# Kernel tuning notes

Hardware: AMD Instinct MI355X
Metric: run time of the kernel (lower is better)

The kernel has to match this reference:

```python
import jax, jax.numpy as jnp
import numpy as np

# Dims: B samples, D=2048 backbone feature dim (resnet50 fc.in_features),
B, D, G, R, K, C = 16384, 2048, 8, 6, 3, 16


def setup_inputs() -> dict:
    key = jax.random.key(0)
    k0, k1, k2, k3 = jax.random.split(key, 4)
    feats = jax.random.normal(k0, (B, D), dtype=jnp.float32)          # backbone output (dropout=eval identity)
    roi_ids = jax.random.randint(k1, (B,), 0, G)                       # per-sample routing id (roi_names)
    W_reg = jax.random.normal(k2, (G, R, D), dtype=jnp.float32) * 0.02  # reg_heads[roi].weight
    b_reg = jnp.zeros((G, R), dtype=jnp.float32)                       # reg_heads[roi].bias
    W_cls = jax.random.normal(k3, (G, K, C, D), dtype=jnp.float32) * 0.02  # cls_heads[roi][k].weight
    b_cls = jnp.zeros((G, K, C), dtype=jnp.float32)                    # cls_heads[roi][k].bias
    return {"feats": feats, "roi_ids": roi_ids, "W_reg": W_reg, "b_reg": b_reg,
            "W_cls": W_cls, "b_cls": b_cls}


def reference(feats, roi_ids, W_reg, b_reg, W_cls, b_cls):
    # Original loop applies, per sample i, the Linear heads of roi_names[i].
    # Vectorized: compute all-ROI head outputs densely, then gather the routed one.
    # (Same math per sample; dropout is identity in eval mode.)
    reg_all = jnp.einsum('bd,grd->bgr', feats, W_reg) + b_reg[None]        # [B, G, R]
    cls_all = jnp.einsum('bd,gkcd->bgkc', feats, W_cls) + b_cls[None]      # [B, G, K, C]
    reg = jnp.take_along_axis(reg_all, roi_ids[:, None, None], axis=1)[:, 0]            # [B, R]
    cls = jnp.take_along_axis(cls_all, roi_ids[:, None, None, None], axis=1)[:, 0]      # [B, K, C]
    return reg, cls
```

## Files before the change

### kernel.cpp

```cpp
#include <hip/hip_runtime.h>
#include <hip/hip_bf16.h>

#define NB   16384
#define ND   2048
#define NG   8
#define NR   6
#define NKC  48
#define NOUT 54
#define BM   32
#define KC3  64
#define NCH3 (ND / KC3)
#define SLOT 16384
#define LROW 136
#define KC   128
#define NCH  (ND / KC)
#define MAXT (NB / BM + NG)

typedef __attribute__((ext_vector_type(8))) short short8_t;
typedef __attribute__((ext_vector_type(4))) float f32x4;

__device__ __forceinline__ unsigned short f2bf(float x) {
    union { float f; unsigned u; } v; v.f = x;
    unsigned r = v.u + 0x7FFFu + ((v.u >> 16) & 1u);
    return (unsigned short)(r >> 16);
}

__device__ __forceinline__ short8_t cvt8(float4 a, float4 b) {
    short8_t s;
    s[0] = (short)f2bf(a.x); s[1] = (short)f2bf(a.y);
    s[2] = (short)f2bf(a.z); s[3] = (short)f2bf(a.w);
    s[4] = (short)f2bf(b.x); s[5] = (short)f2bf(b.y);
    s[6] = (short)f2bf(b.z); s[7] = (short)f2bf(b.w);
    return s;
}

__device__ __forceinline__ void gl_lds16(const void* g, void* s) {
    __builtin_amdgcn_global_load_lds(
        (const __attribute__((address_space(1))) void*)g,
        (__attribute__((address_space(3))) void*)s,
        16, 0, 0);
}

#define WAITV(N) do { asm volatile("s_waitcnt vmcnt(" #N ")" ::: "memory"); \
                      __builtin_amdgcn_sched_barrier(0); } while (0)
#define BARRIER() do { __builtin_amdgcn_s_barrier(); \
                       __builtin_amdgcn_sched_barrier(0); } while (0)

__global__ void hist_kernel(const int* __restrict__ roi, int* __restrict__ counts) {
    int i = blockIdx.x * 256 + threadIdx.x;
    int g = roi[i];
    int lane = threadIdx.x & 63;
    #pragma unroll
    for (int gg = 0; gg < NG; ++gg) {
        unsigned long long m = __ballot(g == gg);
        if (m && lane == (int)(__ffsll((unsigned long long)m) - 1))
            atomicAdd(&counts[gg], (int)__popcll(m));
    }
}

__global__ void scatter_kernel(const int* __restrict__ roi, const int* __restrict__ counts,
                               int* __restrict__ ranks, int* __restrict__ perm) {
    int off[NG];
    int acc = 0;
    #pragma unroll
    for (int gg = 0; gg < NG; ++gg) { off[gg] = acc; acc += counts[gg]; }
    int i = blockIdx.x * 256 + threadIdx.x;
    int g = roi[i];
    int lane = threadIdx.x & 63;
    #pragma unroll
    for (int gg = 0; gg < NG; ++gg) {
        unsigned long long m = __ballot(g == gg);
        if (!m) continue;
        int leader = (int)(__ffsll((unsigned long long)m) - 1);
        int base = 0;
        if (lane == leader) base = atomicAdd(&ranks[gg], (int)__popcll(m));
        base = __shfl(base, leader);
        if (g == gg) {
            int rank = (int)__popcll(m & ((1ull << lane) - 1ull));
            perm[off[gg] + base + rank] = i;
        }
    }
}

__global__ void scatter1_kernel(const int* __restrict__ roi, int* __restrict__ cnt,
                                int* __restrict__ perm) {
    int i = blockIdx.x * 256 + threadIdx.x;
    int g = roi[i];
    int lane = threadIdx.x & 63;
    #pragma unroll
    for (int gg = 0; gg < NG; ++gg) {
        unsigned long long m = __ballot(g == gg);
        if (!m) continue;
        int leader = (int)(__ffsll((unsigned long long)m) - 1);
        int base = 0;
        if (lane == leader) base = atomicAdd(&cnt[gg], (int)__popcll(m));
        base = __shfl(base, leader);
        if (g == gg) {
            int rank = (int)__popcll(m & ((1ull << lane) - 1ull));
            perm[gg * NB + base + rank] = i;
        }
    }
}

__global__ void wconv_kernel(const float* __restrict__ Wreg, const float* __restrict__ Wcls,
                             short* __restrict__ Wbf) {
    int u = blockIdx.x * 256 + threadIdx.x;
    int l  = u & 63;
    int ks = (u >> 6) & 1;
    int n  = (u >> 7) & 1;
    int nh = (u >> 8) & 1;
    int c  = (u >> 9) & 31;
    int g  = u >> 14;
    int row = nh * 32 + n * 16 + (l & 15);
    int k   = c * 64 + ks * 32 + (l >> 4) * 8;
    short8_t v = {0, 0, 0, 0, 0, 0, 0, 0};
    if (row < NOUT) {
        const float* s = (row < NR) ? Wreg + (size_t)(g * NR + row) * ND + k
                                    : Wcls + (size_t)(g * NKC + row - NR) * ND + k;
        float4 a = *(const float4*)s;
        float4 b = *(const float4*)(s + 4);
        v = cvt8(a, b);
    }
    *(short8_t*)(Wbf + (size_t)u * 8) = v;
}

__launch_bounds__(256, 2)
__global__ void gemm_p3_kernel(const float* __restrict__ feats,
                               const short* __restrict__ Wbf,
                               const float* __restrict__ breg, const float* __restrict__ bcls,
                               const int* __restrict__ counts, const int* __restrict__ perm,
                               float* __restrict__ out, int stride) {
    __shared__ __align__(16) char lds[3][SLOT];
    __shared__ int sRow[BM];

    int ts[NG + 1]; ts[0] = 0;
    int off[NG]; int acc_ = 0;
    #pragma unroll
    for (int gg = 0; gg < NG; ++gg) {
        int c = counts[gg];
        off[gg] = stride ? gg * stride : acc_;
        acc_ += c;
        ts[gg + 1] = ts[gg] + (c + BM - 1) / BM;
    }
    int b = blockIdx.x;
    if (b >= ts[NG]) return;
    int g = 0;
    #pragma unroll
    for (int gg = 0; gg < NG; ++gg) if (b >= ts[gg + 1]) g = gg + 1;
    int gcnt  = counts[g];
    int goff  = off[g];
    int rbase = (b - ts[g]) * BM;
    int nvalid = gcnt - rbase; if (nvalid > BM) nvalid = BM;

    int tid = threadIdx.x;
    if (tid < BM) {
        int r = rbase + tid;
        if (r >= gcnt) r = gcnt - 1;
        sRow[tid] = perm[goff + r];
    }
    __syncthreads();

    int w = tid >> 6, l = tid & 63, lr = l & 15, lq = l >> 4;
    int mt = w & 1, nh = w >> 1;

    const float* paBase = feats + (size_t)sRow[mt * 16 + lr] * ND + nh * 32 + lq * 8;
    char* ldsA = &lds[0][0] + (mt * 4096 + nh * 2048);
    const short* pbBase = Wbf + ((size_t)g * 32 * 8 + (nh * 2 + mt) * 2) * 512 + l * 8;
    char* ldsB = &lds[0][8192] + (nh * 4096 + mt * 2048);

#define STAGE(cc, sl) do {                                                     \
        const float* a_ = paBase + (size_t)(cc) * KC3;                         \
        gl_lds16(a_,     ldsA + (sl) * SLOT);                                  \
        gl_lds16(a_ + 4, ldsA + (sl) * SLOT + 1024);                           \
        const short* b_ = pbBase + (size_t)(cc) * 4096;                        \
        gl_lds16(b_,       ldsB + (sl) * SLOT);                                \
        gl_lds16(b_ + 512, ldsB + (sl) * SLOT + 1024);                         \
    } while (0)

    f32x4 acc0 = {0, 0, 0, 0}, acc1 = {0, 0, 0, 0};

    STAGE(0, 0); STAGE(1, 1);

    #pragma unroll
    for (int c = 0; c < NCH3; ++c) {
        const int sl = c % 3;
        if (c + 2 < NCH3) STAGE(c + 2, (c + 2) % 3);
        if (c < NCH3 - 2)       WAITV(8);
        else if (c == NCH3 - 2) WAITV(4);
        else                    WAITV(0);
        BARRIER();
        {
            const char* sa = &lds[sl][mt * 4096];
            const char* sb = &lds[sl][8192 + nh * 4096];
            #pragma unroll
            for (int ks = 0; ks < 2; ++ks) {
                float4 a0 = *(const float4*)(sa + ks * 2048 + l * 16);
                float4 a1 = *(const float4*)(sa + ks * 2048 + 1024 + l * 16);
                short8_t af = cvt8(a0, a1);
                short8_t b0 = *(const short8_t*)(sb + ks * 1024 + l * 16);
                short8_t b1 = *(const short8_t*)(sb + 2048 + ks * 1024 + l * 16);
                acc0 = __builtin_amdgcn_mfma_f32_16x16x32_bf16(af, b0, acc0, 0, 0, 0);
                acc1 = __builtin_amdgcn_mfma_f32_16x16x32_bf16(af, b1, acc1, 0, 0, 0);
            }
        }
        BARRIER();
    }
#undef STAGE

    const int B6 = NB * NR;
    #pragma unroll
    for (int n = 0; n < 2; ++n) {
        f32x4 v = n ? acc1 : acc0;
        int col = nh * 32 + n * 16 + lr;
        if (col < NOUT) {
            #pragma unroll
            for (int j = 0; j < 4; ++j) {
                int row = mt * 16 + lq * 4 + j;
                if (row < nvalid) {
                    int smp = sRow[row];
                    if (col < NR) out[smp * NR + col] = v[j] + breg[g * NR + col];
                    else          out[B6 + smp * NKC + (col - NR)] = v[j] + bcls[g * NKC + (col - NR)];
                }
            }
        }
    }
}

__launch_bounds__(256, 3)
__global__ void gemm_kernel(const float* __restrict__ feats,
                            const float* __restrict__ Wreg, const float* __restrict__ breg,
                            const float* __restrict__ Wcls, const float* __restrict__ bcls,
                            const int* __restrict__ counts, const int* __restrict__ perm,
                            float* __restrict__ out, int stride) {
    __shared__ __align__(16) short Bsh[2][64][LROW];
    __shared__ int sRow[BM];

    int ts[NG + 1]; ts[0] = 0;
    int off[NG]; int acc = 0;
    #pragma unroll
    for (int gg = 0; gg < NG; ++gg) {
        int c = counts[gg];
        off[gg] = stride ? gg * stride : acc;
        acc += c;
        ts[gg + 1] = ts[gg] + (c + BM - 1) / BM;
    }
    int b = blockIdx.x;
    if (b >= ts[NG]) return;
    int g = 0;
    #pragma unroll
    for (int gg = 0; gg < NG; ++gg) if (b >= ts[gg + 1]) g = gg + 1;
    int gcnt  = counts[g];
    int goff  = off[g];
    int rbase = (b - ts[g]) * BM;
    int nvalid = gcnt - rbase; if (nvalid > BM) nvalid = BM;

    int tid = threadIdx.x;
    if (tid < BM) {
        int r = rbase + tid;
        if (r >= gcnt) r = gcnt - 1;
        sRow[tid] = perm[goff + r];
    }
    __syncthreads();

    int rB = tid >> 2;
    int cq = tid & 3;
    const float* wsrc = nullptr;
    if (rB < NR)        wsrc = Wreg + ((size_t)g * NR + rB) * ND + cq * 32;
    else if (rB < NOUT) wsrc = Wcls + ((size_t)g * NKC + (rB - NR)) * ND + cq * 32;

    int w = tid >> 6, l = tid & 63, lr = l & 15, lq = l >> 4;
    int mt = w & 1, nh = w >> 1;
    const float* aptr = feats + (size_t)sRow[mt * 16 + lr] * ND + lq * 8;
    const short* brp = (const short*)&Bsh[0][0][0] + (nh * 32 + lr) * LROW + lq * 8;

    f32x4 acc0 = {0, 0, 0, 0}, acc1 = {0, 0, 0, 0};
    float4 rb[8];

    if (wsrc) {
        #pragma unroll
        for (int i = 0; i < 8; ++i) rb[i] = *(const float4*)(wsrc + 4 * i);
    } else {
        #pragma unroll
        for (int i = 0; i < 8; ++i) rb[i] = make_float4(0.f, 0.f, 0.f, 0.f);
    }
    {
        short* bw = &Bsh[0][rB][cq * 32];
        #pragma unroll
        for (int j = 0; j < 4; ++j) *(short8_t*)(bw + 8 * j) = cvt8(rb[2 * j], rb[2 * j + 1]);
    }
    __syncthreads();

    #pragma unroll
    for (int c = 0; c < NCH; ++c) {
        const int cur = c & 1, nxt = cur ^ 1;
        if (c + 1 < NCH && wsrc) {
            const float* s = wsrc + (c + 1) * KC;
            #pragma unroll
            for (int i = 0; i < 8; ++i) rb[i] = *(const float4*)(s + 4 * i);
        }
        const short* bp = brp + cur * (64 * LROW);
        const float* ap = aptr + c * KC;
        #pragma unroll
        for (int ks = 0; ks < 4; ++ks) {
            float4 a0 = *(const float4*)(ap + ks * 32);
            float4 a1 = *(const float4*)(ap + ks * 32 + 4);
            short8_t af = cvt8(a0, a1);
            short8_t b0 = *(const short8_t*)(bp + ks * 32);
            short8_t b1 = *(const short8_t*)(bp + 16 * LROW + ks * 32);
            acc0 = __builtin_amdgcn_mfma_f32_16x16x32_bf16(af, b0, acc0, 0, 0, 0);
            acc1 = __builtin_amdgcn_mfma_f32_16x16x32_bf16(af, b1, acc1, 0, 0, 0);
        }
        if (c + 1 < NCH && wsrc) {
            short* bw = &Bsh[nxt][rB][cq * 32];
            #pragma unroll
            for (int j = 0; j < 4; ++j) *(short8_t*)(bw + 8 * j) = cvt8(rb[2 * j], rb[2 * j + 1]);
        } else if (c + 1 < NCH) {
            short8_t z = {0,0,0,0,0,0,0,0};
            short* bw = &Bsh[nxt][rB][cq * 32];
            #pragma unroll
            for (int j = 0; j < 4; ++j) *(short8_t*)(bw + 8 * j) = z;
        }
        __syncthreads();
    }

    const int B6 = NB * NR;
    #pragma unroll
    for (int n = 0; n < 2; ++n) {
        f32x4 v = n ? acc1 : acc0;
        int col = nh * 32 + n * 16 + lr;
        if (col < NOUT) {
            #pragma unroll
            for (int j = 0; j < 4; ++j) {
                int row = mt * 16 + lq * 4 + j;
                if (row < nvalid) {
                    int smp = sRow[row];
                    if (col < NR) out[smp * NR + col] = v[j] + breg[g * NR + col];
                    else          out[B6 + smp * NKC + (col - NR)] = v[j] + bcls[g * NKC + (col - NR)];
                }
            }
        }
    }
}

__global__ void fallback_kernel(const float* __restrict__ feats, const int* __restrict__ roi,
                                const float* __restrict__ Wreg, const float* __restrict__ breg,
                                const float* __restrict__ Wcls, const float* __restrict__ bcls,
                                float* __restrict__ out) {
    int i = blockIdx.x;
    int lane = threadIdx.x;
    int g = roi[i];
    const float* frow = feats + (size_t)i * ND;
    float f[32];
    #pragma unroll
    for (int q = 0; q < 32; ++q) f[q] = frow[lane + 64 * q];
    for (int o = 0; o < NOUT; ++o) {
        const float* wrow = (o < NR) ? Wreg + ((size_t)g * NR + o) * ND
                                     : Wcls + ((size_t)g * NKC + (o - NR)) * ND;
        float p = 0.f;
        #pragma unroll
        for (int q = 0; q < 32; ++q) p += f[q] * wrow[lane + 64 * q];
        #pragma unroll
        for (int s = 32; s; s >>= 1) p += __shfl_xor(p, s);
        if (lane == 0) {
            if (o < NR) out[i * NR + o] = p + breg[g * NR + o];
            else        out[NB * NR + i * NKC + (o - NR)] = p + bcls[g * NKC + (o - NR)];
        }
    }
}

extern "C" void kernel_launch(void* const* d_in, const int* in_sizes, int n_in,
                              void* d_out, int out_size, void* d_ws, size_t ws_size,
                              hipStream_t stream) {
    const float* feats = (const float*)d_in[0];
    const int*   roi   = (const int*)d_in[1];
    const float* Wreg  = (const float*)d_in[2];
    const float* breg  = (const float*)d_in[3];
    const float* Wcls  = (const float*)d_in[4];
    const float* bcls  = (const float*)d_in[5];
    float* out = (float*)d_out;

    const size_t wbfBytes = (size_t)NG * 131072 * 2;
    const size_t need_t1 = wbfBytes + 256 + (size_t)NG * NB * 4;
    const size_t need_t3 = 256 + (size_t)NB * 4;

    if (ws_size >= need_t1) {
        short* Wbf = (short*)d_ws;
        int* cnt  = (int*)((char*)d_ws + wbfBytes);
        int* perm = cnt + 64;
        hipMemsetAsync(cnt, 0, 8 * sizeof(int), stream);
        wconv_kernel<<<512, 256, 0, stream>>>(Wreg, Wcls, Wbf);
        scatter1_kernel<<<NB / 256, 256, 0, stream>>>(roi, cnt, perm);
        gemm_p3_kernel<<<MAXT, 256, 0, stream>>>(feats, Wbf, breg, bcls, cnt, perm, out, NB);
    } else if (ws_size >= need_t3) {
        int* counts = (int*)d_ws;
        int* ranks  = counts + 8;
        int* perm   = counts + 64;
        hipMemsetAsync(counts, 0, 16 * sizeof(int), stream);
        hist_kernel<<<NB / 256, 256, 0, stream>>>(roi, counts);
        scatter_kernel<<<NB / 256, 256, 0, stream>>>(roi, counts, ranks, perm);
        gemm_kernel<<<MAXT, 256, 0, stream>>>(feats, Wreg, breg, Wcls, bcls, counts, perm, out, 0);
    } else {
        fallback_kernel<<<NB, 64, 0, stream>>>(feats, roi, Wreg, breg, Wcls, bcls, out);
    }
}
```

Before: 69.91 us.

## Fuse prep kernels and use persistent work-queue GEMM with 64-row tiles

Merges the routing scatter and weight bf16 conversion into one prep kernel, cutting one launch. Replaces the per-tile GEMM grid with a persistent 512-block kernel of 512 threads. Each block pulls 64-row tiles from an atomic queue head and stages A through XOR-swizzled LDS to avoid bank conflicts. This aims to reduce launch overhead and tail imbalance and to improve reuse of the B tile, at the cost of larger LDS use and an atomic per tile.

```diff
diff --git a/kernel.cpp b/kernel.cpp
--- a/kernel.cpp
+++ b/kernel.cpp
@@ -7,11 +7,8 @@
 #define NR   6
 #define NKC  48
 #define NOUT 54
+#define LROW 136
 #define BM   32
-#define KC3  64
-#define NCH3 (ND / KC3)
-#define SLOT 16384
-#define LROW 136
 #define KC   128
 #define NCH  (ND / KC)
 #define MAXT (NB / BM + NG)
@@ -43,8 +40,8 @@
 
 #define WAITV(N) do { asm volatile("s_waitcnt vmcnt(" #N ")" ::: "memory"); \
                       __builtin_amdgcn_sched_barrier(0); } while (0)
-#define BARRIER() do { __builtin_amdgcn_s_barrier(); \
-                       __builtin_amdgcn_sched_barrier(0); } while (0)
+#define BAR() do { __builtin_amdgcn_s_barrier(); \
+                   __builtin_amdgcn_sched_barrier(0); } while (0)
 
 __global__ void hist_kernel(const int* __restrict__ roi, int* __restrict__ counts) {
     int i = blockIdx.x * 256 + threadIdx.x;
@@ -82,64 +79,176 @@
     }
 }
 
-__global__ void scatter1_kernel(const int* __restrict__ roi, int* __restrict__ cnt,
-                                int* __restrict__ perm) {
-    int i = blockIdx.x * 256 + threadIdx.x;
-    int g = roi[i];
-    int lane = threadIdx.x & 63;
-    #pragma unroll
-    for (int gg = 0; gg < NG; ++gg) {
-        unsigned long long m = __ballot(g == gg);
-        if (!m) continue;
-        int leader = (int)(__ffsll((unsigned long long)m) - 1);
-        int base = 0;
-        if (lane == leader) base = atomicAdd(&cnt[gg], (int)__popcll(m));
-        base = __shfl(base, leader);
-        if (g == gg) {
-            int rank = (int)__popcll(m & ((1ull << lane) - 1ull));
-            perm[gg * NB + base + rank] = i;
-        }
-    }
-}
-
-__global__ void wconv_kernel(const float* __restrict__ Wreg, const float* __restrict__ Wcls,
-                             short* __restrict__ Wbf) {
-    int u = blockIdx.x * 256 + threadIdx.x;
-    int l  = u & 63;
-    int ks = (u >> 6) & 1;
-    int n  = (u >> 7) & 1;
-    int nh = (u >> 8) & 1;
-    int c  = (u >> 9) & 31;
-    int g  = u >> 14;
-    int row = nh * 32 + n * 16 + (l & 15);
-    int k   = c * 64 + ks * 32 + (l >> 4) * 8;
-    short8_t v = {0, 0, 0, 0, 0, 0, 0, 0};
-    if (row < NOUT) {
-        const float* s = (row < NR) ? Wreg + (size_t)(g * NR + row) * ND + k
-                                    : Wcls + (size_t)(g * NKC + row - NR) * ND + k;
-        float4 a = *(const float4*)s;
-        float4 b = *(const float4*)(s + 4);
-        v = cvt8(a, b);
-    }
-    *(short8_t*)(Wbf + (size_t)u * 8) = v;
-}
-
-__launch_bounds__(256, 2)
-__global__ void gemm_p3_kernel(const float* __restrict__ feats,
-                               const short* __restrict__ Wbf,
-                               const float* __restrict__ breg, const float* __restrict__ bcls,
-                               const int* __restrict__ counts, const int* __restrict__ perm,
-                               float* __restrict__ out, int stride) {
-    __shared__ __align__(16) char lds[3][SLOT];
+__global__ void prep_kernel(const int* __restrict__ roi, int* __restrict__ cnt,
+                            int* __restrict__ perm,
+                            const float* __restrict__ Wreg, const float* __restrict__ Wcls,
+                            short* __restrict__ Wbf) {
+    if (blockIdx.x < 64) {
+        int i = blockIdx.x * 256 + threadIdx.x;
+        int g = roi[i];
+        int lane = threadIdx.x & 63;
+        #pragma unroll
+        for (int gg = 0; gg < NG; ++gg) {
+            unsigned long long m = __ballot(g == gg);
+            if (!m) continue;
+            int leader = (int)(__ffsll((unsigned long long)m) - 1);
+            int base = 0;
+            if (lane == leader) base = atomicAdd(&cnt[gg], (int)__popcll(m));
+            base = __shfl(base, leader);
+            if (g == gg) {
+                int rank = (int)__popcll(m & ((1ull << lane) - 1ull));
+                perm[gg * NB + base + rank] = i;
+            }
+        }
+    } else {
+        int u = (blockIdx.x - 64) * 256 + threadIdx.x;
+        int l = u & 63;
+        int q = (u >> 6) & 7;
+        int c = (u >> 9) & 31;
+        int g = u >> 14;
+        int nh = q >> 2, nf = (q >> 1) & 1, ks = q & 1;
+        int row = nh * 32 + nf * 16 + (l & 15);
+        int k   = c * 64 + ks * 32 + (l >> 4) * 8;
+        short8_t v = {0, 0, 0, 0, 0, 0, 0, 0};
+        if (row < NOUT) {
+            const float* s = (row < NR) ? Wreg + (size_t)(g * NR + row) * ND + k
+                                        : Wcls + (size_t)(g * NKC + row - NR) * ND + k;
+            float4 a = *(const float4*)s;
+            float4 b = *(const float4*)(s + 4);
+            v = cvt8(a, b);
+        }
+        *(short8_t*)(Wbf + (size_t)u * 8) = v;
+    }
+}
+
+__launch_bounds__(512, 4)
+__global__ void gemm_q_kernel(const float* __restrict__ feats,
+                              const short* __restrict__ Wbf,
+                              const float* __restrict__ breg, const float* __restrict__ bcls,
+                              const int* __restrict__ cnt, const int* __restrict__ perm,
+                              int* __restrict__ qhead, float* __restrict__ out) {
+    __shared__ __align__(16) char lds[3][24576];
+    __shared__ int sRow[64];
+    __shared__ int sTile;
+
+    int tid = threadIdx.x, w = tid >> 6, l = tid & 63, lr = l & 15, lq = l >> 4;
+    int mt = w >> 1, nh = w & 1;
+
+    int ts[NG + 1]; ts[0] = 0;
+    #pragma unroll
+    for (int gg = 0; gg < NG; ++gg) ts[gg + 1] = ts[gg] + ((cnt[gg] + 63) >> 6);
+    const int Ttot = ts[NG];
+
+    const int key   = lr & 7;
+    const int rbyt  = mt * 4096 + lr * 256;
+    const int o00 = (((lq * 2 + 0) ^ key) << 4);
+    const int o01 = (((lq * 2 + 1) ^ key) << 4);
+    const int o10 = (((8 + lq * 2 + 0) ^ key) << 4);
+    const int o11 = (((8 + lq * 2 + 1) ^ key) << 4);
+    const int r0 = (2 * w + 0) * 4 + lq;
+    const int r1 = (2 * w + 1) * 4 + lq;
+    const int sp0 = (((l & 15) ^ (r0 & 7)) << 4);
+    const int sp1 = (((l & 15) ^ (r1 & 7)) << 4);
+    const int B6 = NB * NR;
+
+    for (;;) {
+        if (tid == 0) sTile = atomicAdd(qhead, 1);
+        __syncthreads();
+        int t = sTile;
+        if (t >= Ttot) break;
+
+        int g = 0;
+        #pragma unroll
+        for (int gg = 0; gg < NG; ++gg) if (t >= ts[gg + 1]) g = gg + 1;
+        int cg = cnt[g];
+        int rbase = (t - ts[g]) * 64;
+        int nv = cg - rbase; if (nv > 64) nv = 64;
+
+        if (tid < 64) {
+            int r = rbase + tid;
+            if (r >= cg) r = cg - 1;
+            sRow[tid] = perm[g * NB + r];
+        }
+        __syncthreads();
+
+        const char* a0c = (const char*)(feats + (size_t)sRow[r0] * ND) + sp0;
+        const char* a1c = (const char*)(feats + (size_t)sRow[r1] * ND) + sp1;
+        const char* bB  = (const char*)Wbf + (size_t)g * 262144 + w * 1024 + l * 16;
+
+#define STAGE(cc, sl) do {                                                     \
+        size_t co_ = (size_t)(cc) * 256;                                       \
+        gl_lds16(a0c + co_, &lds[sl][w * 2048]);                               \
+        gl_lds16(a1c + co_, &lds[sl][w * 2048 + 1024]);                        \
+        gl_lds16(bB + (size_t)(cc) * 8192, &lds[sl][16384 + w * 1024]);        \
+    } while (0)
+
+#define CSTEP(ks, o_0, o_1) do {                                               \
+        const char* Ab_ = &lds[csl][0] + rbyt;                                 \
+        const char* Bb_ = &lds[csl][16384] + nh * 4096 + (ks) * 1024 + l * 16; \
+        float4 x0 = *(const float4*)(Ab_ + (ks) * 0 + o_0);                    \
+        float4 x1 = *(const float4*)(Ab_ + o_1);                               \
+        short8_t af = cvt8(x0, x1);                                            \
+        short8_t b0 = *(const short8_t*)(Bb_);                                 \
+        short8_t b1 = *(const short8_t*)(Bb_ + 2048);                          \
+        acc0 = __builtin_amdgcn_mfma_f32_16x16x32_bf16(af, b0, acc0, 0, 0, 0); \
+        acc1 = __builtin_amdgcn_mfma_f32_16x16x32_bf16(af, b1, acc1, 0, 0, 0); \
+    } while (0)
+
+        f32x4 acc0 = {0, 0, 0, 0}, acc1 = {0, 0, 0, 0};
+
+        STAGE(0, 0); STAGE(1, 1);
+        int csl = 0;
+        #pragma unroll
+        for (int c = 0; c < 32; ++c) {
+            if (c + 2 < 32) STAGE(c + 2, (c + 2) % 3);
+            if (c < 30)       WAITV(6);
+            else if (c == 30) WAITV(3);
+            else              WAITV(0);
+            BAR();
+            CSTEP(0, o00, o01);
+            CSTEP(1, o10, o11);
+            BAR();
+            csl = (csl == 2) ? 0 : csl + 1;
+        }
+#undef STAGE
+#undef CSTEP
+
+        #pragma unroll
+        for (int n = 0; n < 2; ++n) {
+            f32x4 v = n ? acc1 : acc0;
+            int col = nh * 32 + n * 16 + lr;
+            if (col < NOUT) {
+                #pragma unroll
+                for (int j = 0; j < 4; ++j) {
+                    int row = mt * 16 + lq * 4 + j;
+                    if (row < nv) {
+                        int smp = sRow[row];
+                        if (col < NR) out[smp * NR + col] = v[j] + breg[g * NR + col];
+                        else          out[B6 + smp * NKC + (col - NR)] = v[j] + bcls[g * NKC + (col - NR)];
+                    }
+                }
+            }
+        }
+        __syncthreads();
+    }
+}
+
+__launch_bounds__(256, 3)
+__global__ void gemm_kernel(const float* __restrict__ feats,
+                            const float* __restrict__ Wreg, const float* __restrict__ breg,
+                            const float* __restrict__ Wcls, const float* __restrict__ bcls,
+                            const int* __restrict__ counts, const int* __restrict__ perm,
+                            float* __restrict__ out, int stride) {
+    __shared__ __align__(16) short Bsh[2][64][LROW];
     __shared__ int sRow[BM];
 
     int ts[NG + 1]; ts[0] = 0;
-    int off[NG]; int acc_ = 0;
+    int off[NG]; int acc = 0;
     #pragma unroll
     for (int gg = 0; gg < NG; ++gg) {
         int c = counts[gg];
-        off[gg] = stride ? gg * stride : acc_;
-        acc_ += c;
+        off[gg] = stride ? gg * stride : acc;
+        acc += c;
         ts[gg + 1] = ts[gg] + (c + BM - 1) / BM;
     }
     int b = blockIdx.x;
@@ -160,52 +269,66 @@
     }
     __syncthreads();
 
+    int rB = tid >> 2;
+    int cq = tid & 3;
+    const float* wsrc = nullptr;
+    if (rB < NR)        wsrc = Wreg + ((size_t)g * NR + rB) * ND + cq * 32;
+    else if (rB < NOUT) wsrc = Wcls + ((size_t)g * NKC + (rB - NR)) * ND + cq * 32;
+
     int w = tid >> 6, l = tid & 63, lr = l & 15, lq = l >> 4;
     int mt = w & 1, nh = w >> 1;
-
-    const float* paBase = feats + (size_t)sRow[mt * 16 + lr] * ND + nh * 32 + lq * 8;
-    char* ldsA = &lds[0][0] + (mt * 4096 + nh * 2048);
-    const short* pbBase = Wbf + ((size_t)g * 32 * 8 + (nh * 2 + mt) * 2) * 512 + l * 8;
-    char* ldsB = &lds[0][8192] + (nh * 4096 + mt * 2048);
-
-#define STAGE(cc, sl) do {                                                     \
-        const float* a_ = paBase + (size_t)(cc) * KC3;                         \
-        gl_lds16(a_,     ldsA + (sl) * SLOT);                                  \
-        gl_lds16(a_ + 4, ldsA + (sl) * SLOT + 1024);                           \
-        const short* b_ = pbBase + (size_t)(cc) * 4096;                        \
-        gl_lds16(b_,       ldsB + (sl) * SLOT);                                \
-        gl_lds16(b_ + 512, ldsB + (sl) * SLOT + 1024);                         \
-    } while (0)
+    const float* aptr = feats + (size_t)sRow[mt * 16 + lr] * ND + lq * 8;
+    const short* brp = (const short*)&Bsh[0][0][0] + (nh * 32 + lr) * LROW + lq * 8;
 
     f32x4 acc0 = {0, 0, 0, 0}, acc1 = {0, 0, 0, 0};
-
-    STAGE(0, 0); STAGE(1, 1);
-
-    #pragma unroll
-    for (int c = 0; c < NCH3; ++c) {
-        const int sl = c % 3;
-        if (c + 2 < NCH3) STAGE(c + 2, (c + 2) % 3);
-        if (c < NCH3 - 2)       WAITV(8);
-        else if (c == NCH3 - 2) WAITV(4);
-        else                    WAITV(0);
-        BARRIER();
-        {
-            const char* sa = &lds[sl][mt * 4096];
-            const char* sb = &lds[sl][8192 + nh * 4096];
+    float4 rb[8];
+
+    if (wsrc) {
+        #pragma unroll
+        for (int i = 0; i < 8; ++i) rb[i] = *(const float4*)(wsrc + 4 * i);
+    } else {
+        #pragma unroll
+        for (int i = 0; i < 8; ++i) rb[i] = make_float4(0.f, 0.f, 0.f, 0.f);
+    }
+    {
+        short* bw = &Bsh[0][rB][cq * 32];
+        #pragma unroll
+        for (int j = 0; j < 4; ++j) *(short8_t*)(bw + 8 * j) = cvt8(rb[2 * j], rb[2 * j + 1]);
+    }
+    __syncthreads();
+
+    #pragma unroll
+    for (int c = 0; c < NCH; ++c) {
+        const int cur = c & 1, nxt = cur ^ 1;
+        if (c + 1 < NCH && wsrc) {
+            const float* s = wsrc + (c + 1) * KC;
             #pragma unroll
-            for (int ks = 0; ks < 2; ++ks) {
-                float4 a0 = *(const float4*)(sa + ks * 2048 + l * 16);
-                float4 a1 = *(const float4*)(sa + ks * 2048 + 1024 + l * 16);
-                short8_t af = cvt8(a0, a1);
-                short8_t b0 = *(const short8_t*)(sb + ks * 1024 + l * 16);
-                short8_t b1 = *(const short8_t*)(sb + 2048 + ks * 1024 + l * 16);
-                acc0 = __builtin_amdgcn_mfma_f32_16x16x32_bf16(af, b0, acc0, 0, 0, 0);
-                acc1 = __builtin_amdgcn_mfma_f32_16x16x32_bf16(af, b1, acc1, 0, 0, 0);
-            }
-        }
-        BARRIER();
-    }
-#undef STAGE
+            for (int i = 0; i < 8; ++i) rb[i] = *(const float4*)(s + 4 * i);
+        }
+        const short* bp = brp + cur * (64 * LROW);
+        const float* ap = aptr + c * KC;
+        #pragma unroll
+        for (int ks = 0; ks < 4; ++ks) {
+            float4 a0 = *(const float4*)(ap + ks * 32);
+            float4 a1 = *(const float4*)(ap + ks * 32 + 4);
+            short8_t af = cvt8(a0, a1);
+            short8_t b0 = *(const short8_t*)(bp + ks * 32);
+            short8_t b1 = *(const short8_t*)(bp + 16 * LROW + ks * 32);
+            acc0 = __builtin_amdgcn_mfma_f32_16x16x32_bf16(af, b0, acc0, 0, 0, 0);
+            acc1 = __builtin_amdgcn_mfma_f32_16x16x32_bf16(af, b1, acc1, 0, 0, 0);
+        }
+        if (c + 1 < NCH && wsrc) {
+            short* bw = &Bsh[nxt][rB][cq * 32];
+            #pragma unroll
+            for (int j = 0; j < 4; ++j) *(short8_t*)(bw + 8 * j) = cvt8(rb[2 * j], rb[2 * j + 1]);
+        } else if (c + 1 < NCH) {
+            short8_t z = {0,0,0,0,0,0,0,0};
+            short* bw = &Bsh[nxt][rB][cq * 32];
+            #pragma unroll
+            for (int j = 0; j < 4; ++j) *(short8_t*)(bw + 8 * j) = z;
+        }
+        __syncthreads();
+    }
 
     const int B6 = NB * NR;
     #pragma unroll
@@ -226,122 +349,6 @@
     }
 }
 
-__launch_bounds__(256, 3)
-__global__ void gemm_kernel(const float* __restrict__ feats,
-                            const float* __restrict__ Wreg, const float* __restrict__ breg,
-                            const float* __restrict__ Wcls, const float* __restrict__ bcls,
-                            const int* __restrict__ counts, const int* __restrict__ perm,
-                            float* __restrict__ out, int stride) {
-    __shared__ __align__(16) short Bsh[2][64][LROW];
-    __shared__ int sRow[BM];
-
-    int ts[NG + 1]; ts[0] = 0;
-    int off[NG]; int acc = 0;
-    #pragma unroll
-    for (int gg = 0; gg < NG; ++gg) {
-        int c = counts[gg];
-        off[gg] = stride ? gg * stride : acc;
-        acc += c;
-        ts[gg + 1] = ts[gg] + (c + BM - 1) / BM;
-    }
-    int b = blockIdx.x;
-    if (b >= ts[NG]) return;
-    int g = 0;
-    #pragma unroll
-    for (int gg = 0; gg < NG; ++gg) if (b >= ts[gg + 1]) g = gg + 1;
-    int gcnt  = counts[g];
-    int goff  = off[g];
-    int rbase = (b - ts[g]) * BM;
-    int nvalid = gcnt - rbase; if (nvalid > BM) nvalid = BM;
-
-    int tid = threadIdx.x;
-    if (tid < BM) {
-        int r = rbase + tid;
-        if (r >= gcnt) r = gcnt - 1;
-        sRow[tid] = perm[goff + r];
-    }
-    __syncthreads();
-
-    int rB = tid >> 2;
-    int cq = tid & 3;
-    const float* wsrc = nullptr;
-    if (rB < NR)        wsrc = Wreg + ((size_t)g * NR + rB) * ND + cq * 32;
-    else if (rB < NOUT) wsrc = Wcls + ((size_t)g * NKC + (rB - NR)) * ND + cq * 32;
-
-    int w = tid >> 6, l = tid & 63, lr = l & 15, lq = l >> 4;
-    int mt = w & 1, nh = w >> 1;
-    const float* aptr = feats + (size_t)sRow[mt * 16 + lr] * ND + lq * 8;
-    const short* brp = (const short*)&Bsh[0][0][0] + (nh * 32 + lr) * LROW + lq * 8;
-
-    f32x4 acc0 = {0, 0, 0, 0}, acc1 = {0, 0, 0, 0};
-    float4 rb[8];
-
-    if (wsrc) {
-        #pragma unroll
-        for (int i = 0; i < 8; ++i) rb[i] = *(const float4*)(wsrc + 4 * i);
-    } else {
-        #pragma unroll
-        for (int i = 0; i < 8; ++i) rb[i] = make_float4(0.f, 0.f, 0.f, 0.f);
-    }
-    {
-        short* bw = &Bsh[0][rB][cq * 32];
-        #pragma unroll
-        for (int j = 0; j < 4; ++j) *(short8_t*)(bw + 8 * j) = cvt8(rb[2 * j], rb[2 * j + 1]);
-    }
-    __syncthreads();
-
-    #pragma unroll
-    for (int c = 0; c < NCH; ++c) {
-        const int cur = c & 1, nxt = cur ^ 1;
-        if (c + 1 < NCH && wsrc) {
-            const float* s = wsrc + (c + 1) * KC;
-            #pragma unroll
-            for (int i = 0; i < 8; ++i) rb[i] = *(const float4*)(s + 4 * i);
-        }
-        const short* bp = brp + cur * (64 * LROW);
-        const float* ap = aptr + c * KC;
-        #pragma unroll
-        for (int ks = 0; ks < 4; ++ks) {
-            float4 a0 = *(const float4*)(ap + ks * 32);
-            float4 a1 = *(const float4*)(ap + ks * 32 + 4);
-            short8_t af = cvt8(a0, a1);
-            short8_t b0 = *(const short8_t*)(bp + ks * 32);
-            short8_t b1 = *(const short8_t*)(bp + 16 * LROW + ks * 32);
-            acc0 = __builtin_amdgcn_mfma_f32_16x16x32_bf16(af, b0, acc0, 0, 0, 0);
-            acc1 = __builtin_amdgcn_mfma_f32_16x16x32_bf16(af, b1, acc1, 0, 0, 0);
-        }
-        if (c + 1 < NCH && wsrc) {
-            short* bw = &Bsh[nxt][rB][cq * 32];
-            #pragma unroll
-            for (int j = 0; j < 4; ++j) *(short8_t*)(bw + 8 * j) = cvt8(rb[2 * j], rb[2 * j + 1]);
-        } else if (c + 1 < NCH) {
-            short8_t z = {0,0,0,0,0,0,0,0};
-            short* bw = &Bsh[nxt][rB][cq * 32];
-            #pragma unroll
-            for (int j = 0; j < 4; ++j) *(short8_t*)(bw + 8 * j) = z;
-        }
-        __syncthreads();
-    }
-
-    const int B6 = NB * NR;
-    #pragma unroll
-    for (int n = 0; n < 2; ++n) {
-        f32x4 v = n ? acc1 : acc0;
-        int col = nh * 32 + n * 16 + lr;
-        if (col < NOUT) {
-            #pragma unroll
-            for (int j = 0; j < 4; ++j) {
-                int row = mt * 16 + lq * 4 + j;
-                if (row < nvalid) {
-                    int smp = sRow[row];
-                    if (col < NR) out[smp * NR + col] = v[j] + breg[g * NR + col];
-                    else          out[B6 + smp * NKC + (col - NR)] = v[j] + bcls[g * NKC + (col - NR)];
-                }
-            }
-        }
-    }
-}
-
 __global__ void fallback_kernel(const float* __restrict__ feats, const int* __restrict__ roi,
                                 const float* __restrict__ Wreg, const float* __restrict__ breg,
                                 const float* __restrict__ Wcls, const float* __restrict__ bcls,
@@ -385,12 +392,12 @@
 
     if (ws_size >= need_t1) {
         short* Wbf = (short*)d_ws;
-        int* cnt  = (int*)((char*)d_ws + wbfBytes);
-        int* perm = cnt + 64;
-        hipMemsetAsync(cnt, 0, 8 * sizeof(int), stream);
-        wconv_kernel<<<512, 256, 0, stream>>>(Wreg, Wcls, Wbf);
-        scatter1_kernel<<<NB / 256, 256, 0, stream>>>(roi, cnt, perm);
-        gemm_p3_kernel<<<MAXT, 256, 0, stream>>>(feats, Wbf, breg, bcls, cnt, perm, out, NB);
+        int* cnt   = (int*)((char*)d_ws + wbfBytes);
+        int* qhead = cnt + 8;
+        int* perm  = cnt + 64;
+        hipMemsetAsync(cnt, 0, 64, stream);
+        prep_kernel<<<576, 256, 0, stream>>>(roi, cnt, perm, Wreg, Wcls, Wbf);
+        gemm_q_kernel<<<512, 512, 0, stream>>>(feats, Wbf, breg, bcls, cnt, perm, qhead, out);
     } else if (ws_size >= need_t3) {
         int* counts = (int*)d_ws;
         int* ranks  = counts + 8;
```

Result: no change. 69.74 us (-0.2%).
